# Kernel tuning notes

Hardware: AMD Instinct MI355X
Metric: run time of the kernel (lower is better)

The kernel has to match this reference:

```python
import jax, jax.numpy as jnp
import numpy as np

B, S, D, H, DK, DV, DFF, L, V = 8, 1024, 256, 8, 32, 32, 1024, 4, 28
EPS = 1e-5
NEG = -1e9


def _ln(x, w, b):
    m = jnp.mean(x, axis=-1, keepdims=True)
    v = jnp.var(x, axis=-1, keepdims=True)
    return (x - m) * jax.lax.rsqrt(v + EPS) * w + b


def setup_inputs() -> dict:
    key = jax.random.key(0)
    ks = jax.random.split(key, 30)
    std = 0.02
    inp = {
        'input_ids': jax.random.randint(ks[0], (B, S), 0, V),
        'tok_embed': jax.random.normal(ks[1], (V, D), jnp.float32) * std,
        'pos_embed': jax.random.normal(ks[2], (S, D), jnp.float32) * std,
        'emb_ln_w': jnp.ones((D,), jnp.float32),
        'emb_ln_b': jnp.zeros((D,), jnp.float32),
        'Wq': jax.random.normal(ks[3], (L, D, H * DK), jnp.float32) * std,
        'bq': jnp.zeros((L, H * DK), jnp.float32),
        'Wk': jax.random.normal(ks[4], (L, D, H * DK), jnp.float32) * std,
        'bk': jnp.zeros((L, H * DK), jnp.float32),
        'Wv': jax.random.normal(ks[5], (L, D, H * DV), jnp.float32) * std,
        'bv': jnp.zeros((L, H * DV), jnp.float32),
        'Wo': jax.random.normal(ks[6], (L, H * DV, D), jnp.float32) * std,
        'bo': jnp.zeros((L, D), jnp.float32),
        'ln_w': jnp.ones((L, D), jnp.float32),
        'ln_b': jnp.zeros((L, D), jnp.float32),
        'W1': jax.random.normal(ks[7], (L, D, DFF), jnp.float32) * std,
        'b1': jnp.zeros((L, DFF), jnp.float32),
        'W2': jax.random.normal(ks[8], (L, DFF, D), jnp.float32) * std,
        'b2': jnp.zeros((L, D), jnp.float32),
        'ft1_w': jax.random.normal(ks[9], (D, D), jnp.float32) * std,
        'ft1_b': jnp.zeros((D,), jnp.float32),
        'ft2_w': jax.random.normal(ks[10], (D, D // 2), jnp.float32) * std,
        'ft2_b': jnp.zeros((D // 2,), jnp.float32),
        'cls_w': jax.random.normal(ks[11], (D // 2, 2), jnp.float32) * std,
        'cls_b': jnp.zeros((2,), jnp.float32),
    }
    return inp


def reference(input_ids, tok_embed, pos_embed, emb_ln_w, emb_ln_b,
              Wq, bq, Wk, bk, Wv, bv, Wo, bo, ln_w, ln_b,
              W1, b1, W2, b2, ft1_w, ft1_b, ft2_w, ft2_b, cls_w, cls_b):
    # Embedding: tok + pos, then LayerNorm
    x = tok_embed[input_ids] + pos_embed[jnp.arange(S)][None, :, :]
    x = _ln(x, emb_ln_w, emb_ln_b)
    # pad mask: True where key position is pad (token id 0); broadcast [B,1,1,S]
    pad = (input_ids == 0)[:, None, None, :]
    scale = 1.0 / np.sqrt(DK)
    for i in range(L):
        residual = x
        q = (x @ Wq[i] + bq[i]).reshape(B, S, H, DK).transpose(0, 2, 1, 3)
        k = (x @ Wk[i] + bk[i]).reshape(B, S, H, DK).transpose(0, 2, 1, 3)
        v = (x @ Wv[i] + bv[i]).reshape(B, S, H, DV).transpose(0, 2, 1, 3)
        scores = jnp.einsum('bhqd,bhkd->bhqk', q, k) * scale
        scores = jnp.where(pad, NEG, scores)
        attn = jax.nn.softmax(scores, axis=-1)
        ctx = jnp.einsum('bhqk,bhkd->bhqd', attn, v)
        ctx = ctx.transpose(0, 2, 1, 3).reshape(B, S, H * DV)
        x = _ln(ctx @ Wo[i] + bo[i] + residual, ln_w[i], ln_b[i])
        # FFN (note: original has NO residual/norm after FFN)
        x = jax.nn.relu(x @ W1[i] + b1[i]) @ W2[i] + b2[i]
    cls = x[:, 0, :]
    feat = jax.nn.relu(cls @ ft1_w + ft1_b) @ ft2_w + ft2_b  # dropout = eval no-op
    logits = feat @ cls_w + cls_b
    return logits, feat
```

## Files before the change

### kernel.cpp

```cpp
#include <hip/hip_runtime.h>
#include <math.h>

#define S_ 1024
#define D_ 256

typedef __attribute__((ext_vector_type(8))) _Float16 half8;
typedef __attribute__((ext_vector_type(4))) _Float16 half4;
typedef __attribute__((ext_vector_type(2))) _Float16 half2v;
typedef __attribute__((ext_vector_type(4))) float f32x4;
typedef __attribute__((ext_vector_type(4))) unsigned int u32x4;

__device__ __forceinline__ float wave_sum64(float x) {
    x += __shfl_xor(x, 32); x += __shfl_xor(x, 16); x += __shfl_xor(x, 8);
    x += __shfl_xor(x, 4);  x += __shfl_xor(x, 2);  x += __shfl_xor(x, 1);
    return x;
}

#define GLD16(gp, lp) __builtin_amdgcn_global_load_lds( \
    (const __attribute__((address_space(1))) void*)(gp), \
    (__attribute__((address_space(3))) void*)(lp), 16, 0, 0)

__global__ __launch_bounds__(256) void transpose_cvt(
    const float* __restrict__ src, _Float16* __restrict__ dst, int K, int N)
{
    __shared__ float tile[32][33];
    src += (size_t)blockIdx.z * K * N;
    dst += (size_t)blockIdx.z * K * N;
    const int bx = blockIdx.x * 32;
    const int by = blockIdx.y * 32;
    const int t = threadIdx.x;
    const int c = t & 31, r0 = t >> 5;
    #pragma unroll
    for (int j = 0; j < 4; ++j)
        tile[r0 + 8 * j][c] = src[(size_t)(by + r0 + 8 * j) * N + bx + c];
    __syncthreads();
    #pragma unroll
    for (int j = 0; j < 4; ++j)
        dst[(size_t)(bx + r0 + 8 * j) * K + by + c] = (_Float16)tile[c][r0 + 8 * j];
}

__global__ __launch_bounds__(256) void transpose_qkv(
    const float* __restrict__ Wq, const float* __restrict__ Wk,
    const float* __restrict__ Wv, _Float16* __restrict__ qkvT)
{
    __shared__ float tile[32][33];
    const int z = blockIdx.z, l = z / 3, m = z % 3;
    const float* src = (m == 0 ? Wq : (m == 1 ? Wk : Wv)) + (size_t)l * 65536;
    _Float16* dst = qkvT + (size_t)l * 196608 + (size_t)m * 65536;
    const int bx = blockIdx.x * 32;
    const int by = blockIdx.y * 32;
    const int t = threadIdx.x;
    const int c = t & 31, r0 = t >> 5;
    #pragma unroll
    for (int j = 0; j < 4; ++j)
        tile[r0 + 8 * j][c] = src[(size_t)(by + r0 + 8 * j) * 256 + bx + c];
    __syncthreads();
    #pragma unroll
    for (int j = 0; j < 4; ++j)
        dst[(size_t)(bx + r0 + 8 * j) * 256 + by + c] = (_Float16)tile[c][r0 + 8 * j];
}

__global__ __launch_bounds__(256) void pack_bias(
    const float* __restrict__ bq, const float* __restrict__ bk,
    const float* __restrict__ bv, float* __restrict__ bqkv)
{
    const int z = blockIdx.x, l = z / 3, m = z % 3;
    const float* s = (m == 0 ? bq : (m == 1 ? bk : bv)) + l * 256;
    bqkv[l * 768 + m * 256 + threadIdx.x] = s[threadIdx.x];
}

__global__ __launch_bounds__(256) void embed_ln_kernel(
    const int* __restrict__ ids, const float* __restrict__ tok,
    const float* __restrict__ pos, const float* __restrict__ w,
    const float* __restrict__ b, float* __restrict__ X, _Float16* __restrict__ Xh)
{
    const int wv_ = threadIdx.x >> 6, lane = threadIdx.x & 63;
    const int tokid = blockIdx.x * 4 + wv_;
    const int s = tokid & (S_ - 1);
    const int id = ids[tokid];
    float4 e = *(const float4*)&tok[id * D_ + lane * 4];
    float4 p = *(const float4*)&pos[s * D_ + lane * 4];
    float4 x = make_float4(e.x + p.x, e.y + p.y, e.z + p.z, e.w + p.w);
    float sum = x.x + x.y + x.z + x.w;
    float sq  = x.x * x.x + x.y * x.y + x.z * x.z + x.w * x.w;
    sum = wave_sum64(sum); sq = wave_sum64(sq);
    float mean = sum * (1.f / D_);
    float var  = sq * (1.f / D_) - mean * mean;
    float rs   = rsqrtf(var + 1e-5f);
    float4 wv = *(const float4*)&w[lane * 4];
    float4 bv = *(const float4*)&b[lane * 4];
    float4 o = make_float4((x.x - mean) * rs * wv.x + bv.x,
                           (x.y - mean) * rs * wv.y + bv.y,
                           (x.z - mean) * rs * wv.z + bv.z,
                           (x.w - mean) * rs * wv.w + bv.w);
    *(float4*)&X[(size_t)tokid * D_ + lane * 4] = o;
    half4 oh = { (_Float16)o.x, (_Float16)o.y, (_Float16)o.z, (_Float16)o.w };
    *(half4*)&Xh[(size_t)tokid * D_ + lane * 4] = oh;
}

__global__ __launch_bounds__(256) void ln_kernel(
    const float* __restrict__ Y, const float* __restrict__ w,
    const float* __restrict__ b, _Float16* __restrict__ Th)
{
    const int wv_ = threadIdx.x >> 6, lane = threadIdx.x & 63;
    const int tokid = blockIdx.x * 4 + wv_;
    const size_t base = (size_t)tokid * D_ + lane * 4;
    float4 x = *(const float4*)&Y[base];
    float sum = x.x + x.y + x.z + x.w;
    float sq  = x.x * x.x + x.y * x.y + x.z * x.z + x.w * x.w;
    sum = wave_sum64(sum); sq = wave_sum64(sq);
    float mean = sum * (1.f / D_);
    float var  = sq * (1.f / D_) - mean * mean;
    float rs   = rsqrtf(var + 1e-5f);
    float4 wv = *(const float4*)&w[lane * 4];
    float4 bv = *(const float4*)&b[lane * 4];
    half4 oh = { (_Float16)((x.x - mean) * rs * wv.x + bv.x),
                 (_Float16)((x.y - mean) * rs * wv.y + bv.y),
                 (_Float16)((x.z - mean) * rs * wv.z + bv.z),
                 (_Float16)((x.w - mean) * rs * wv.w + bv.w) };
    *(half4*)&Th[base] = oh;
}

template<int MODE>
__global__ __launch_bounds__(256) void gemm_f16(
    const _Float16* __restrict__ A, const _Float16* __restrict__ Bt,
    const float* __restrict__ bias, const float* __restrict__ res,
    float* __restrict__ Cf, _Float16* __restrict__ Ch,
    int K, int N)
{
    __shared__ _Float16 As[2][8192];
    const int t = threadIdx.x;
    const int wid = t >> 6, lane = t & 63;
    const int wr = wid >> 1, wc = wid & 1;
    const int m0 = blockIdx.x * 128, n0 = blockIdx.y * 64;
    const int li = lane & 15, lg = lane >> 4;
    const int srow = lane >> 3;
    const int scg = (lane & 7) ^ srow;

    f32x4 acc[4][2];
    const f32x4 zf = {0.f, 0.f, 0.f, 0.f};
    #pragma unroll
    for (int mr = 0; mr < 4; ++mr) { acc[mr][0] = zf; acc[mr][1] = zf; }

    const int KT = K >> 6;
    {
        const _Float16* Ab = A + (size_t)m0 * K;
        #pragma unroll
        for (int j = 0; j < 4; ++j) {
            int row = (wid * 4 + j) * 8 + srow;
            GLD16(Ab + (size_t)row * K + scg * 8, &As[0][(wid * 4 + j) * 512]);
        }
    }

    for (int kt = 0; kt < KT; ++kt) {
        const int cur = kt & 1;
        half8 bfr[2][2];
        #pragma unroll
        for (int nr = 0; nr < 2; ++nr) {
            const _Float16* bp = Bt + (size_t)(n0 + wc * 32 + nr * 16 + li) * K + kt * 64 + lg * 8;
            bfr[nr][0] = *(const half8*)bp;
            bfr[nr][1] = *(const half8*)(bp + 32);
        }
        if (kt + 1 < KT) {
            const _Float16* Ab = A + (size_t)m0 * K + (kt + 1) * 64;
            #pragma unroll
            for (int j = 0; j < 4; ++j) {
                int row = (wid * 4 + j) * 8 + srow;
                GLD16(Ab + (size_t)row * K + scg * 8, &As[cur ^ 1][(wid * 4 + j) * 512]);
            }
            asm volatile("s_waitcnt vmcnt(8)" ::: "memory");
        } else {
            asm volatile("s_waitcnt vmcnt(4)" ::: "memory");
        }
        __builtin_amdgcn_s_barrier();
        #pragma unroll
        for (int kk = 0; kk < 2; ++kk) {
            half8 af[4];
            #pragma unroll
            for (int mr = 0; mr < 4; ++mr) {
                int arow = wr * 64 + mr * 16 + li;
                int ablk = (kk * 4 + lg) ^ (li & 7);
                af[mr] = *(const half8*)&As[cur][arow * 64 + ablk * 8];
            }
            #pragma unroll
            for (int mr = 0; mr < 4; ++mr)
                #pragma unroll
                for (int nr = 0; nr < 2; ++nr)
                    acc[mr][nr] = __builtin_amdgcn_mfma_f32_16x16x32_f16(
                        af[mr], bfr[nr][kk], acc[mr][nr], 0, 0, 0);
        }
        __builtin_amdgcn_s_barrier();
    }

    #pragma unroll
    for (int nr = 0; nr < 2; ++nr) {
        const int n = n0 + wc * 32 + nr * 16 + li;
        const float bv = bias[n];
        #pragma unroll
        for (int mr = 0; mr < 4; ++mr) {
            #pragma unroll
            for (int r = 0; r < 4; ++r) {
                const int m = m0 + wr * 64 + mr * 16 + lg * 4 + r;
                float o = acc[mr][nr][r] + bv;
                if (MODE == 1) o = fmaxf(o, 0.f);
                if (MODE == 4) o += res[(size_t)m * N + n];
                if (MODE == 0 || MODE == 2 || MODE == 4) Cf[(size_t)m * N + n] = o;
                if (MODE == 1 || MODE == 2 || MODE == 3) Ch[(size_t)m * N + n] = (_Float16)o;
            }
        }
    }
}

__global__ __launch_bounds__(256, 4) void attn_f16_kernel(
    const _Float16* __restrict__ qkv, const int* __restrict__ ids,
    _Float16* __restrict__ ctxo)
{
    __shared__ unsigned int VTp[32 * 36];
    __shared__ float maskn[64];
    const int t = threadIdx.x;
    const int bh = blockIdx.x, b = bh >> 3, h = bh & 7;
    const int q0 = blockIdx.y * 64;
    const int wid = t >> 6;
    const int lane = t & 63;
    const int i = lane & 15;
    const int g = lane >> 4;
    const int kp = t >> 3;
    const int v0s = (t & 7) * 4;

    const size_t bS = (size_t)b * S_;
    const float scale = 0.17677669529663687f * 1.4426950408889634f;

    const half8 qf = *(const half8*)(qkv + (bS + q0 + wid * 16 + i) * 768 + h * 32 + g * 8);

    float m = -INFINITY, l = 0.f;
    f32x4 cacc[2];
    const f32x4 zf = {0.f, 0.f, 0.f, 0.f};
    cacc[0] = zf; cacc[1] = zf;

    const _Float16* kbase = qkv + 256 + (bS + i) * 768 + h * 32 + g * 8;
    const _Float16* vbase = qkv + 512 + (bS + 2 * kp) * 768 + h * 32 + v0s;

    for (int kt = 0; kt < 16; ++kt) {
        const int k0 = kt * 64;
        {
            const ushort* vb = (const ushort*)(vbase + (size_t)k0 * 768);
            ushort4 a0 = *(const ushort4*)vb;
            ushort4 a1 = *(const ushort4*)(vb + 768);
            VTp[(v0s + 0) * 36 + kp] = (unsigned)a0.x | ((unsigned)a1.x << 16);
            VTp[(v0s + 1) * 36 + kp] = (unsigned)a0.y | ((unsigned)a1.y << 16);
            VTp[(v0s + 2) * 36 + kp] = (unsigned)a0.z | ((unsigned)a1.z << 16);
            VTp[(v0s + 3) * 36 + kp] = (unsigned)a0.w | ((unsigned)a1.w << 16);
            if (t < 64) maskn[t] = (ids[bS + k0 + t] == 0) ? -1e9f : 0.f;
        }
        half8 kf[4];
        const _Float16* kb = kbase + (size_t)k0 * 768;
        #pragma unroll
        for (int c = 0; c < 4; ++c) kf[c] = *(const half8*)(kb + c * 16 * 768);
        f32x4 sacc[4];
        #pragma unroll
        for (int c = 0; c < 4; ++c)
            sacc[c] = __builtin_amdgcn_mfma_f32_16x16x32_f16(kf[c], qf, zf, 0, 0, 0);
        __syncthreads();
        float p[4][4];
        float tmax = -INFINITY;
        #pragma unroll
        for (int c = 0; c < 4; ++c) {
            float4 ad = *(const float4*)&maskn[c * 16 + g * 4];
            p[c][0] = fmaf(sacc[c][0], scale, ad.x);
            p[c][1] = fmaf(sacc[c][1], scale, ad.y);
            p[c][2] = fmaf(sacc[c][2], scale, ad.z);
            p[c][3] = fmaf(sacc[c][3], scale, ad.w);
            tmax = fmaxf(tmax, fmaxf(fmaxf(p[c][0], p[c][1]), fmaxf(p[c][2], p[c][3])));
        }
        tmax = fmaxf(tmax, __shfl_xor(tmax, 16));
        tmax = fmaxf(tmax, __shfl_xor(tmax, 32));
        if (__any(tmax > m)) {
            float mn  = fmaxf(m, tmax);
            float fac = exp2f(m - mn);
            l *= fac;
            cacc[0] *= fac;
            cacc[1] *= fac;
            m = mn;
        }
        float psum = 0.f;
        #pragma unroll
        for (int c = 0; c < 4; ++c) {
            p[c][0] = exp2f(p[c][0] - m); p[c][1] = exp2f(p[c][1] - m);
            p[c][2] = exp2f(p[c][2] - m); p[c][3] = exp2f(p[c][3] - m);
            psum += (p[c][0] + p[c][1]) + (p[c][2] + p[c][3]);
        }
        psum += __shfl_xor(psum, 16);
        psum += __shfl_xor(psum, 32);
        l += psum;
        #pragma unroll
        for (int c = 0; c < 4; ++c) {
            half2v plo = __builtin_bit_cast(half2v, __builtin_amdgcn_cvt_pkrtz(p[c][0], p[c][1]));
            half2v phi = __builtin_bit_cast(half2v, __builtin_amdgcn_cvt_pkrtz(p[c][2], p[c][3]));
            half4 pb = { plo[0], plo[1], phi[0], phi[1] };
            #pragma unroll
            for (int vh = 0; vh < 2; ++vh) {
                const unsigned int* vp = &VTp[(vh * 16 + i) * 36 + 8 * c + 2 * g];
                unsigned long long vv = *(const unsigned long long*)vp;
                half4 vf = __builtin_bit_cast(half4, vv);
                cacc[vh] = __builtin_amdgcn_mfma_f32_16x16x16f16(vf, pb, cacc[vh], 0, 0, 0);
            }
        }
        __syncthreads();
    }
    const float inv = 1.f / l;
    _Float16* crow = ctxo + (bS + q0 + wid * 16 + i) * 256 + h * 32;
    #pragma unroll
    for (int vh = 0; vh < 2; ++vh) {
        half4 st;
        #pragma unroll
        for (int r = 0; r < 4; ++r) st[r] = (_Float16)(cacc[vh][r] * inv);
        *(half4*)&crow[vh * 16 + g * 4] = st;
    }
}

__global__ __launch_bounds__(256) void head1_kernel(
    const float* __restrict__ X, const float* __restrict__ ft1w,
    const float* __restrict__ ft1b, float* __restrict__ h1)
{
    __shared__ float clsS[8][256];
    __shared__ float ps[8][8][32];
    const int t = threadIdx.x;
    #pragma unroll
    for (int b = 0; b < 8; ++b) clsS[b][t] = X[(size_t)b * S_ * D_ + t];
    __syncthreads();
    const int n = t & 31, dg = t >> 5;
    const int gn = blockIdx.x * 32 + n;
    float s[8] = {};
    for (int dd = 0; dd < 32; ++dd) {
        int d = dg * 32 + dd;
        float w = ft1w[d * 256 + gn];
        #pragma unroll
        for (int b = 0; b < 8; ++b) s[b] = fmaf(clsS[b][d], w, s[b]);
    }
    #pragma unroll
    for (int b = 0; b < 8; ++b) ps[dg][b][n] = s[b];
    __syncthreads();
    {
        const int b = t >> 5, nn = t & 31;
        float a = 0.f;
        #pragma unroll
        for (int g = 0; g < 8; ++g) a += ps[g][b][nn];
        const int gn2 = blockIdx.x * 32 + nn;
        h1[b * 256 + gn2] = fmaxf(a + ft1b[gn2], 0.f);
    }
}

__global__ __launch_bounds__(256) void head2_kernel(
    const float* __restrict__ h1, const float* __restrict__ ft2w,
    const float* __restrict__ ft2b, float* __restrict__ featW,
    float* __restrict__ out)
{
    __shared__ float hS[8][256];
    __shared__ float ps[8][8][32];
    const int t = threadIdx.x;
    #pragma unroll
    for (int b = 0; b < 8; ++b) hS[b][t] = h1[b * 256 + t];
    __syncthreads();
    const int n = t & 31, dg = t >> 5;
    const int gn = blockIdx.x * 32 + n;
    float s[8] = {};
    for (int dd = 0; dd < 32; ++dd) {
        int d = dg * 32 + dd;
        float w = ft2w[d * 128 + gn];
        #pragma unroll
        for (int b = 0; b < 8; ++b) s[b] = fmaf(hS[b][d], w, s[b]);
    }
    #pragma unroll
    for (int b = 0; b < 8; ++b) ps[dg][b][n] = s[b];
    __syncthreads();
    {
        const int b = t >> 5, nn = t & 31;
        float a = 0.f;
        #pragma unroll
        for (int g = 0; g < 8; ++g) a += ps[g][b][nn];
        const int gn2 = blockIdx.x * 32 + nn;
        float v = a + ft2b[gn2];
        featW[b * 128 + gn2] = v;
        out[16 + b * 128 + gn2] = v;
    }
}

__global__ __launch_bounds__(64) void head3_kernel(
    const float* __restrict__ featW, const float* __restrict__ clw,
    const float* __restrict__ clb, float* __restrict__ out)
{
    const int t = threadIdx.x;
    if (t < 16) {
        const int b = t >> 1, c = t & 1;
        float s = 0.f;
        for (int d = 0; d < 128; ++d) s = fmaf(featW[b * 128 + d], clw[d * 2 + c], s);
        out[t] = s + clb[c];
    }
}

extern "C" void kernel_launch(void* const* d_in, const int* in_sizes, int n_in,
                              void* d_out, int out_size, void* d_ws, size_t ws_size,
                              hipStream_t stream)
{
    const int*   ids  = (const int*)d_in[0];
    const float* tok  = (const float*)d_in[1];
    const float* pos  = (const float*)d_in[2];
    const float* elnw = (const float*)d_in[3];
    const float* elnb = (const float*)d_in[4];
    const float* Wq   = (const float*)d_in[5];
    const float* bq   = (const float*)d_in[6];
    const float* Wk   = (const float*)d_in[7];
    const float* bk   = (const float*)d_in[8];
    const float* Wv   = (const float*)d_in[9];
    const float* bv   = (const float*)d_in[10];
    const float* Wo   = (const float*)d_in[11];
    const float* bo   = (const float*)d_in[12];
    const float* lnw  = (const float*)d_in[13];
    const float* lnb  = (const float*)d_in[14];
    const float* W1   = (const float*)d_in[15];
    const float* b1   = (const float*)d_in[16];
    const float* W2   = (const float*)d_in[17];
    const float* b2   = (const float*)d_in[18];
    const float* ft1w = (const float*)d_in[19];
    const float* ft1b = (const float*)d_in[20];
    const float* ft2w = (const float*)d_in[21];
    const float* ft2b = (const float*)d_in[22];
    const float* clw  = (const float*)d_in[23];
    const float* clb  = (const float*)d_in[24];
    float* out = (float*)d_out;

    char* ws = (char*)d_ws;
    float*    X    = (float*)(ws);
    float*    Y    = (float*)(ws + (8ull << 20));
    _Float16* Xh   = (_Float16*)(ws + (16ull << 20));
    _Float16* Th   = (_Float16*)(ws + (20ull << 20));
    _Float16* qkvb = (_Float16*)(ws + (24ull << 20));
    _Float16* ctx  = (_Float16*)(ws + (36ull << 20));
    _Float16* Hb   = (_Float16*)(ws + (24ull << 20));
    _Float16* qkvT = (_Float16*)(ws + (40ull << 20));
    _Float16* WoT  = (_Float16*)(ws + (42ull << 20));
    _Float16* W1T  = (_Float16*)(ws + (43ull << 20));
    _Float16* W2T  = (_Float16*)(ws + (45ull << 20));
    float*    bqkv = (float*)(ws + (47ull << 20));
    float*    h1W  = (float*)(ws + (47ull << 20) + (16ull << 10));
    float*    feW  = (float*)(ws + (47ull << 20) + (24ull << 10));

    transpose_qkv<<<dim3(8, 8, 12), 256, 0, stream>>>(Wq, Wk, Wv, qkvT);
    transpose_cvt<<<dim3(8, 8, 4),  256, 0, stream>>>(Wo, WoT, 256, 256);
    transpose_cvt<<<dim3(32, 8, 4), 256, 0, stream>>>(W1, W1T, 256, 1024);
    transpose_cvt<<<dim3(8, 32, 4), 256, 0, stream>>>(W2, W2T, 1024, 256);
    pack_bias<<<12, 256, 0, stream>>>(bq, bk, bv, bqkv);

    embed_ln_kernel<<<2048, 256, 0, stream>>>(ids, tok, pos, elnw, elnb, X, Xh);

    for (int i = 0; i < 4; ++i) {
        gemm_f16<3><<<dim3(64, 12), 256, 0, stream>>>(
            Xh, qkvT + (size_t)i * 196608, bqkv + i * 768, nullptr, nullptr, qkvb, 256, 768);
        attn_f16_kernel<<<dim3(64, 16), 256, 0, stream>>>(qkvb, ids, ctx);
        gemm_f16<4><<<dim3(64, 4), 256, 0, stream>>>(
            ctx, WoT + (size_t)i * 65536, bo + i * 256, X, Y, nullptr, 256, 256);
        ln_kernel<<<2048, 256, 0, stream>>>(Y, lnw + i * 256, lnb + i * 256, Th);
        gemm_f16<1><<<dim3(64, 16), 256, 0, stream>>>(
            Th, W1T + (size_t)i * 262144, b1 + i * 1024, nullptr, nullptr, Hb, 256, 1024);
        gemm_f16<2><<<dim3(64, 4), 256, 0, stream>>>(
            Hb, W2T + (size_t)i * 262144, b2 + i * 256, nullptr, X, Xh, 1024, 256);
    }

    head1_kernel<<<8, 256, 0, stream>>>(X, ft1w, ft1b, h1W);
    head2_kernel<<<4, 256, 0, stream>>>(h1W, ft2w, ft2b, feW, out);
    head3_kernel<<<1, 64, 0, stream>>>(feW, clw, clb, out);
}
```

Baseline: 446.7 us.

## Double-buffer V tile and pad mask in attention kernel with one barrier per iteration

The attention kernel now keeps two LDS buffers for the transposed V tile and the pad mask. Loads for the next key tile are issued at the top of each iteration and written to the alternate buffer after the softmax, so global latency overlaps with compute. This cuts the barriers per iteration from two to one. The LDS row stride changes from 36 to 38, which shifts bank mapping. In exchange, LDS use and register pressure rise slightly.

```diff
diff --git a/kernel.cpp b/kernel.cpp
--- a/kernel.cpp
+++ b/kernel.cpp
@@ -215,8 +215,8 @@
     const _Float16* __restrict__ qkv, const int* __restrict__ ids,
     _Float16* __restrict__ ctxo)
 {
-    __shared__ unsigned int VTp[32 * 36];
-    __shared__ float maskn[64];
+    __shared__ unsigned int VTp[2][32 * 38];
+    __shared__ float maskn[2][64];
     const int t = threadIdx.x;
     const int bh = blockIdx.x, b = bh >> 3, h = bh & 7;
     const int q0 = blockIdx.y * 64;
@@ -240,18 +240,30 @@
     const _Float16* kbase = qkv + 256 + (bS + i) * 768 + h * 32 + g * 8;
     const _Float16* vbase = qkv + 512 + (bS + 2 * kp) * 768 + h * 32 + v0s;
 
+    {
+        const ushort* vb = (const ushort*)vbase;
+        ushort4 a0 = *(const ushort4*)vb;
+        ushort4 a1 = *(const ushort4*)(vb + 768);
+        VTp[0][(v0s + 0) * 38 + kp] = (unsigned)a0.x | ((unsigned)a1.x << 16);
+        VTp[0][(v0s + 1) * 38 + kp] = (unsigned)a0.y | ((unsigned)a1.y << 16);
+        VTp[0][(v0s + 2) * 38 + kp] = (unsigned)a0.z | ((unsigned)a1.z << 16);
+        VTp[0][(v0s + 3) * 38 + kp] = (unsigned)a0.w | ((unsigned)a1.w << 16);
+        if (t < 64) maskn[0][t] = (ids[bS + t] == 0) ? -1e9f : 0.f;
+    }
+
     for (int kt = 0; kt < 16; ++kt) {
+        const int cur = kt & 1;
+        __syncthreads();
+        ushort4 a0, a1;
+        int midv = 1;
+        const bool have = (kt < 15);
+        if (have) {
+            const ushort* vb = (const ushort*)(vbase + (size_t)(kt + 1) * 64 * 768);
+            a0 = *(const ushort4*)vb;
+            a1 = *(const ushort4*)(vb + 768);
+            if (t < 64) midv = ids[bS + (kt + 1) * 64 + t];
+        }
         const int k0 = kt * 64;
-        {
-            const ushort* vb = (const ushort*)(vbase + (size_t)k0 * 768);
-            ushort4 a0 = *(const ushort4*)vb;
-            ushort4 a1 = *(const ushort4*)(vb + 768);
-            VTp[(v0s + 0) * 36 + kp] = (unsigned)a0.x | ((unsigned)a1.x << 16);
-            VTp[(v0s + 1) * 36 + kp] = (unsigned)a0.y | ((unsigned)a1.y << 16);
-            VTp[(v0s + 2) * 36 + kp] = (unsigned)a0.z | ((unsigned)a1.z << 16);
-            VTp[(v0s + 3) * 36 + kp] = (unsigned)a0.w | ((unsigned)a1.w << 16);
-            if (t < 64) maskn[t] = (ids[bS + k0 + t] == 0) ? -1e9f : 0.f;
-        }
         half8 kf[4];
         const _Float16* kb = kbase + (size_t)k0 * 768;
         #pragma unroll
@@ -260,12 +272,11 @@
         #pragma unroll
         for (int c = 0; c < 4; ++c)
             sacc[c] = __builtin_amdgcn_mfma_f32_16x16x32_f16(kf[c], qf, zf, 0, 0, 0);
-        __syncthreads();
         float p[4][4];
         float tmax = -INFINITY;
         #pragma unroll
         for (int c = 0; c < 4; ++c) {
-            float4 ad = *(const float4*)&maskn[c * 16 + g * 4];
+            float4 ad = *(const float4*)&maskn[cur][c * 16 + g * 4];
             p[c][0] = fmaf(sacc[c][0], scale, ad.x);
             p[c][1] = fmaf(sacc[c][1], scale, ad.y);
             p[c][2] = fmaf(sacc[c][2], scale, ad.z);
@@ -292,6 +303,13 @@
         psum += __shfl_xor(psum, 16);
         psum += __shfl_xor(psum, 32);
         l += psum;
+        if (have) {
+            VTp[cur ^ 1][(v0s + 0) * 38 + kp] = (unsigned)a0.x | ((unsigned)a1.x << 16);
+            VTp[cur ^ 1][(v0s + 1) * 38 + kp] = (unsigned)a0.y | ((unsigned)a1.y << 16);
+            VTp[cur ^ 1][(v0s + 2) * 38 + kp] = (unsigned)a0.z | ((unsigned)a1.z << 16);
+            VTp[cur ^ 1][(v0s + 3) * 38 + kp] = (unsigned)a0.w | ((unsigned)a1.w << 16);
+            if (t < 64) maskn[cur ^ 1][t] = (midv == 0) ? -1e9f : 0.f;
+        }
         #pragma unroll
         for (int c = 0; c < 4; ++c) {
             half2v plo = __builtin_bit_cast(half2v, __builtin_amdgcn_cvt_pkrtz(p[c][0], p[c][1]));
@@ -299,13 +317,12 @@
             half4 pb = { plo[0], plo[1], phi[0], phi[1] };
             #pragma unroll
             for (int vh = 0; vh < 2; ++vh) {
-                const unsigned int* vp = &VTp[(vh * 16 + i) * 36 + 8 * c + 2 * g];
+                const unsigned int* vp = &VTp[cur][(vh * 16 + i) * 38 + 8 * c + 2 * g];
                 unsigned long long vv = *(const unsigned long long*)vp;
                 half4 vf = __builtin_bit_cast(half4, vv);
                 cacc[vh] = __builtin_amdgcn_mfma_f32_16x16x16f16(vf, pb, cacc[vh], 0, 0, 0);
             }
         }
-        __syncthreads();
     }
     const float inv = 1.f / l;
     _Float16* crow = ctxo + (bS + q0 + wid * 16 + i) * 256 + h * 32;
```

Result: no change. 447.3 us (+0.1%).
